# Optimization experiments

Hardware: AMD Instinct MI355X
Metric: run time of the kernel (lower is better)

## Reference

```python
import jax, jax.numpy as jnp
import numpy as np

T, B, Y = 256, 2048, 20   # time, batch, y_dim
H = 256                   # rnn_macro_dim
HD = 256                  # h_dim (decoder MLP)
N_LAYERS = 2


def _gru_cell(x, h, Wih, Whh, bih, bhh):
    # PyTorch GRU cell. Wih: [3H, in], Whh: [3H, H]; gate order r, z, n.
    gx = x @ Wih.T + bih            # [B, 3H]
    gh = h @ Whh.T + bhh            # [B, 3H]
    gx_r, gx_z, gx_n = jnp.split(gx, 3, axis=-1)
    gh_r, gh_z, gh_n = jnp.split(gh, 3, axis=-1)
    r = jax.nn.sigmoid(gx_r + gh_r)
    z = jax.nn.sigmoid(gx_z + gh_z)
    n = jnp.tanh(gx_n + r * gh_n)
    return (1.0 - z) * n + z * h


def setup_inputs() -> dict:
    key = jax.random.key(0)
    ks = jax.random.split(key, 16)
    s = 0.05
    inp = {
        'data': jax.random.normal(ks[0], (T, B, Y), dtype=jnp.float32),
        # GRU layer 0 (input Y) and layer 1 (input H)
        'Wih0': jax.random.normal(ks[1], (3 * H, Y), dtype=jnp.float32) * s,
        'Whh0': jax.random.normal(ks[2], (3 * H, H), dtype=jnp.float32) * s,
        'bih0': jax.random.normal(ks[3], (3 * H,), dtype=jnp.float32) * s,
        'bhh0': jax.random.normal(ks[4], (3 * H,), dtype=jnp.float32) * s,
        'Wih1': jax.random.normal(ks[5], (3 * H, H), dtype=jnp.float32) * s,
        'Whh1': jax.random.normal(ks[6], (3 * H, H), dtype=jnp.float32) * s,
        'bih1': jax.random.normal(ks[7], (3 * H,), dtype=jnp.float32) * s,
        'bhh1': jax.random.normal(ks[8], (3 * H,), dtype=jnp.float32) * s,
        # dec_macro: Linear(H, HD) -> ReLU -> Linear(HD, HD) -> ReLU -> Linear(HD, Y)
        'W1': jax.random.normal(ks[9], (HD, H), dtype=jnp.float32) * s,
        'b1': jax.random.normal(ks[10], (HD,), dtype=jnp.float32) * s,
        'W2': jax.random.normal(ks[11], (HD, HD), dtype=jnp.float32) * s,
        'b2': jax.random.normal(ks[12], (HD,), dtype=jnp.float32) * s,
        'W3': jax.random.normal(ks[13], (Y, HD), dtype=jnp.float32) * s,
        'b3': jax.random.normal(ks[14], (Y,), dtype=jnp.float32) * s,
    }
    return inp


def reference(data, Wih0, Whh0, bih0, bhh0, Wih1, Whh1, bih1, bhh1,
              W1, b1, W2, b2, W3, b3):
    # hp['train'] == 'macro' branch of PROG_RNN_DET.forward
    batch = data.shape[1]
    h_init = jnp.zeros((N_LAYERS, batch, H), dtype=data.dtype)

    def step(h, xs):
        x_t, next_t = xs
        h0 = _gru_cell(x_t, h[0], Wih0, Whh0, bih0, bhh0)
        h1 = _gru_cell(h0, h[1], Wih1, Whh1, bih1, bhh1)
        d = jax.nn.relu(h1 @ W1.T + b1)
        d = jax.nn.relu(d @ W2.T + b2)
        d = d @ W3.T + b3
        loss_t = jnp.sum((d - next_t) ** 2)
        return jnp.stack([h0, h1]), loss_t

    _, losses = jax.lax.scan(step, h_init, (data[:-1], data[1:]))
    return jnp.sum(losses)
```

## Files before the change

kernel.cpp:

```cpp
#include <hip/hip_runtime.h>
#include <stdint.h>

typedef __attribute__((ext_vector_type(4))) float f32x4;
typedef __attribute__((ext_vector_type(2))) long lx2;
typedef unsigned short u16;
typedef unsigned char u8;

#define MFMA8(a,b,c) __builtin_amdgcn_mfma_f32_16x16x32_fp8_fp8((a),(b),(c),0,0,0)

static constexpr int T_STEPS = 256;
static constexpr int BATCH   = 2048;
static constexpr int YDIM    = 20;
static constexpr int BS      = 16;
static constexpr int NWG     = BATCH / BS;

static constexpr int NPAIR   = 768;
static constexpr int WS_U16  = NPAIR * 512;

__device__ __forceinline__ float sigm(float x) { return 1.0f / (1.0f + __expf(-x)); }
__device__ __forceinline__ float tanh_fast(float x) {
    float s = __expf(-2.0f * fabsf(x));
    float r = (1.0f - s) / (1.0f + s);
    return copysignf(r, x);
}
__device__ __forceinline__ f32x4 zero4() { f32x4 v = {0.f,0.f,0.f,0.f}; return v; }
__device__ __forceinline__ u8 f2f8(float v) {
    return (u8)(__builtin_amdgcn_cvt_pk_fp8_f32(v, v, 0, false) & 0xff);
}

__device__ float sval(int P, int half, int l16, int k8,
                      const float* __restrict__ Wih0, const float* __restrict__ Whh0,
                      const float* __restrict__ Wih1, const float* __restrict__ Whh1,
                      const float* __restrict__ W1,   const float* __restrict__ W2,
                      const float* __restrict__ W3) {
    if (P < 192) { int kb=P/24, r=P%24, g=r>>3, wv=r&7, c=wv+8*half;
        return Whh0[(g*256 + c*16 + l16)*256 + kb*32 + k8]; }
    if (P < 224) { int r=P-192; if (r>=24) return 0.f;
        int g=r>>3, wv=r&7, c=wv+8*half, row=g*256+c*16+l16;
        return (k8 < YDIM) ? Wih0[row*YDIM + k8] : 0.f; }
    if (P < 416) { int r=P-224, kb=r/24, rr=r%24, g=rr>>3, wv=rr&7, c=wv+8*half;
        return Whh1[(g*256 + c*16 + l16)*256 + kb*32 + k8]; }
    if (P < 608) { int r=P-416, kb=r/24, rr=r%24, g=rr>>3, wv=rr&7, c=wv+8*half;
        return Wih1[(g*256 + c*16 + l16)*256 + kb*32 + k8]; }
    if (P < 672) { int r=P-608, kb=r>>3, wv=r&7, row=(wv+8*half)*16+l16;
        return W1[row*256 + kb*32 + k8]; }
    if (P < 736) { int r=P-672, kb=r>>3, wv=r&7, row=(wv+8*half)*16+l16;
        return W2[row*256 + kb*32 + k8]; }
    { int r=P-736, s=r>>3, wv=r&7;
      if (wv < 2) { int kb = 2*s + half, row = wv*16 + l16;
          return (row < YDIM) ? W3[row*256 + kb*32 + k8] : 0.f; }
      return 0.f; }
}

__global__ void prep_kernel(const float* __restrict__ Wih0, const float* __restrict__ Whh0,
                            const float* __restrict__ Wih1, const float* __restrict__ Whh1,
                            const float* __restrict__ W1,   const float* __restrict__ W2,
                            const float* __restrict__ W3,   u16* __restrict__ ws,
                            float* __restrict__ out) {
    int tid = blockIdx.x * blockDim.x + threadIdx.x;
    if (tid == 0) out[0] = 0.0f;
    int stride = gridDim.x * blockDim.x;
    for (int m = tid; m < WS_U16; m += stride) {
        int byte0 = 2 * m;
        int P = byte0 >> 10, rem = byte0 & 1023;
        int L = rem >> 4, half = (rem >> 3) & 1, j0 = rem & 7;
        int l16 = L & 15, kqb = (L >> 4) * 8;
        float v0 = sval(P, half, l16, kqb + j0,     Wih0, Whh0, Wih1, Whh1, W1, W2, W3);
        float v1 = sval(P, half, l16, kqb + j0 + 1, Wih0, Whh0, Wih1, Whh1, W1, W2, W3);
        ws[m] = (u16)(__builtin_amdgcn_cvt_pk_fp8_f32(v0, v1, 0, false) & 0xffff);
    }
}

#define BARX() do {                                                 \
    asm volatile("s_waitcnt lgkmcnt(0)" ::: "memory");              \
    __builtin_amdgcn_sched_barrier(0);                              \
    __builtin_amdgcn_s_barrier();                                   \
    __builtin_amdgcn_sched_barrier(0);                              \
} while (0)

#define GM2(ACC, A, PV) do { ACC[0] = MFMA8((A), (PV).x, ACC[0]);   \
                             ACC[1] = MFMA8((A), (PV).y, ACC[1]); } while (0)
#define AFB(S, KT) (*(const long*)&(S)[l16][(KT) * 32 + kq8])
#define LOADC(R0, R1, R2, R3, C) do {                               \
    const u8* b_ = wsl + (size_t)(C) * 32768 + woff;                \
    R0 = *(const lx2*)(b_);          R1 = *(const lx2*)(b_ + 8192); \
    R2 = *(const lx2*)(b_ + 16384); R3 = *(const lx2*)(b_ + 24576); \
} while (0)
#define LP(BASE, P) (*(const lx2*)&(BASE)[(size_t)(P) * 1024 + (size_t)lane * 16])
#define XCH_A(P0,P1,P2,P3, S, KB, AR,AZ,AN) do {                    \
    const long a0_ = AFB(S, KB), a1_ = AFB(S, (KB)+1);              \
    GM2(AR,a0_,P0); GM2(AZ,a0_,P1); GM2(AN,a0_,P2); GM2(AR,a1_,P3); } while (0)
#define XCH_B(P0,P1,P2,P3, S, KB, AR,AZ,AN) do {                    \
    const long a0_ = AFB(S, KB), a1_ = AFB(S, (KB)+1);              \
    GM2(AZ,a0_,P0); GM2(AN,a0_,P1); GM2(AR,a1_,P2); GM2(AZ,a1_,P3); } while (0)
#define XCH_C(P0,P1,P2,P3, S, KB, AR,AZ,AN) do {                    \
    const long a0_ = AFB(S, KB), a1_ = AFB(S, (KB)+1);              \
    GM2(AN,a0_,P0); GM2(AR,a1_,P1); GM2(AZ,a1_,P2); GM2(AN,a1_,P3); } while (0)
#define XCH_M(P0,P1,P2,P3, S, KB0) do {                             \
    const long m0_ = AFB(S, KB0),     m1_ = AFB(S, (KB0)+1);        \
    const long m2_ = AFB(S, (KB0)+2), m3_ = AFB(S, (KB0)+3);        \
    d0 = MFMA8(m0_, P0.x, d0);  d1v = MFMA8(m0_, P0.y, d1v);        \
    d0 = MFMA8(m1_, P1.x, d0);  d1v = MFMA8(m1_, P1.y, d1v);        \
    d0 = MFMA8(m2_, P2.x, d0);  d1v = MFMA8(m2_, P2.y, d1v);        \
    d0 = MFMA8(m3_, P3.x, d0);  d1v = MFMA8(m3_, P3.y, d1v);        \
} while (0)
#define COMBINE(HSH, HR, BRv, BZv, BXNv, BHNv, AR, AZ, AXN, AHN) do {            \
    _Pragma("unroll") for (int jj = 0; jj < 2; ++jj) {                           \
        const int colb_ = (w + 8 * jj) * 16 + l16;                               \
        _Pragma("unroll") for (int q = 0; q < 4; ++q) {                          \
            const float r_ = sigm(AR[jj][q] + BRv[jj]);                          \
            const float z_ = sigm(AZ[jj][q] + BZv[jj]);                          \
            const float n_ = tanh_fast(AXN[jj][q] + BXNv[jj] + r_ * (AHN[jj][q] + BHNv[jj])); \
            const float hn_ = (1.0f - z_) * n_ + z_ * HR[jj][q];                 \
            HR[jj][q] = hn_;                                                     \
            HSH[kq * 4 + q][colb_] = f2f8(hn_); } }                              \
} while (0)
#define DWRITE(DSH, SB) do {                                                     \
    _Pragma("unroll") for (int q = 0; q < 4; ++q) {                              \
        DSH[kq * 4 + q][w * 16 + l16]       = f2f8(fmaxf(d0[q]  + SB[0], 0.f));  \
        DSH[kq * 4 + q][(8 + w) * 16 + l16] = f2f8(fmaxf(d1v[q] + SB[1], 0.f)); }\
} while (0)
#define ZACC(A) do { A[0] = zero4(); A[1] = zero4(); } while (0)

__global__ __launch_bounds__(512, 1) void rnn_main(
    const float* __restrict__ data,
    const float* __restrict__ bih0g, const float* __restrict__ bhh0g,
    const float* __restrict__ bih1g, const float* __restrict__ bhh1g,
    const float* __restrict__ b1g,  const float* __restrict__ b2g,
    const float* __restrict__ b3g,
    const u16* __restrict__ ws, float* __restrict__ out)
{
    __shared__ __align__(16) u8 lds_whh0[3 * 32768];
    __shared__ __align__(16) u8 sh_h0[2][16][272];
    __shared__ __align__(16) u8 sh_h1[2][16][272];
    __shared__ __align__(16) u8 sh_d1[16][272];
    __shared__ __align__(16) u8 sh_d2[16][272];
    __shared__ __align__(16) u8 sh_x[16][32];

    const int tid  = threadIdx.x;
    const int w    = tid >> 6;
    const int lane = tid & 63;
    const int l16  = lane & 15;
    const int kq   = lane >> 4;
    const int kq8  = kq * 8;
    const int b0   = blockIdx.x * BS;
    const int xr   = tid / YDIM, xc = tid - xr * YDIM;
    const size_t woff = (size_t)w * 1024 + (size_t)lane * 16;

    {
        const lx2* s = (const lx2*)ws;
        lx2* dW = (lx2*)lds_whh0;
        for (int i = tid; i < 6144; i += 512) dW[i] = s[i];
    }

    for (int i = tid; i < 2 * 16 * 272; i += 512) { (&sh_h0[0][0][0])[i] = 0; (&sh_h1[0][0][0])[i] = 0; }
    for (int i = tid; i < 16 * 32;  i += 512) (&sh_x[0][0])[i] = 0;
    if (tid < BS * YDIM) sh_x[xr][xc] = f2f8(data[(size_t)b0 * YDIM + tid]);

    float bR0[2], bZ0[2], bXN0[2], bHN0[2], bR1[2], bZ1[2], bXN1[2], bHN1[2], s1r[2], s2r[2];
    #pragma unroll
    for (int jj = 0; jj < 2; ++jj) {
        const int colb = (w + 8 * jj) * 16 + l16;
        bR0[jj]  = bih0g[colb] + bhh0g[colb];
        bZ0[jj]  = bih0g[colb + 256] + bhh0g[colb + 256];
        bXN0[jj] = bih0g[colb + 512];  bHN0[jj] = bhh0g[colb + 512];
        bR1[jj]  = bih1g[colb] + bhh1g[colb];
        bZ1[jj]  = bih1g[colb + 256] + bhh1g[colb + 256];
        bXN1[jj] = bih1g[colb + 512];  bHN1[jj] = bhh1g[colb + 512];
        s1r[jj]  = b1g[colb];  s2r[jj] = b2g[colb];
    }
    float s3r = 0.0f;
    { const int col = w * 16 + l16; if (w < 2 && col < YDIM) s3r = b3g[col]; }

    float hr0[2][4] = {{0,0,0,0},{0,0,0,0}};
    float hr1[2][4] = {{0,0,0,0},{0,0,0,0}};
    f32x4 r0[2], z0[2], xn0[2], hn0[2];
    f32x4 r1[2], z1[2], xn1[2], hn1[2];
    f32x4 d0, d1v;
    lx2 p00, p01, p02, p03, p10, p11, p12, p13, p20, p21, p22, p23;

    __syncthreads();

    {
        const u8* wsl = (const u8*)ws;
        LOADC(p00, p01, p02, p03, 3);
        LOADC(p10, p11, p12, p13, 4);
        LOADC(p20, p21, p22, p23, 5);
    }
    float loss = 0.0f;

    #pragma unroll 1
    for (int t = 0; t < T_STEPS - 1; ++t) {
        const u8* wsl = (const u8*)ws;
        asm volatile("" : "+s"(wsl));
        u8 (*h0o)[272] = sh_h0[t & 1];  u8 (*h0n)[272] = sh_h0[(t & 1) ^ 1];
        u8 (*h1o)[272] = sh_h1[t & 1];  u8 (*h1n)[272] = sh_h1[(t & 1) ^ 1];

        ZACC(r0); ZACC(z0); ZACC(xn0); ZACC(hn0);
        ZACC(r1); ZACC(z1); ZACC(xn1); ZACC(hn1);

        {   lx2 q0=LP(lds_whh0, w),    q1=LP(lds_whh0, 8+w),  q2=LP(lds_whh0, 16+w), q3=LP(lds_whh0, 24+w);
            XCH_A(q0,q1,q2,q3, h0o, 0, r0,z0,hn0); }
        {   lx2 q0=LP(lds_whh0, 32+w), q1=LP(lds_whh0, 40+w), q2=LP(lds_whh0, 48+w), q3=LP(lds_whh0, 56+w);
            XCH_B(q0,q1,q2,q3, h0o, 1, r0,z0,hn0); }
        {   lx2 q0=LP(lds_whh0, 64+w), q1=LP(lds_whh0, 72+w), q2=LP(lds_whh0, 80+w), q3=LP(lds_whh0, 88+w);
            XCH_C(q0,q1,q2,q3, h0o, 2, r0,z0,hn0); }
        XCH_A(p00,p01,p02,p03, h0o, 4, r0,z0,hn0);  LOADC(p00,p01,p02,p03, 6);
        XCH_B(p10,p11,p12,p13, h0o, 5, r0,z0,hn0);  LOADC(p10,p11,p12,p13, 7);
        XCH_C(p20,p21,p22,p23, h0o, 6, r0,z0,hn0);  LOADC(p20,p21,p22,p23, 8);
        {
            const long ax = *(const long*)&sh_x[l16][kq8];
            GM2(r0, ax, p00); GM2(z0, ax, p01); GM2(xn0, ax, p02);
        }
        LOADC(p00,p01,p02,p03, 9);
        XCH_A(p10,p11,p12,p13, h1o, 0, r1,z1,hn1);  LOADC(p10,p11,p12,p13, 10);
        XCH_B(p20,p21,p22,p23, h1o, 1, r1,z1,hn1);  LOADC(p20,p21,p22,p23, 11);
        XCH_C(p00,p01,p02,p03, h1o, 2, r1,z1,hn1);  LOADC(p00,p01,p02,p03, 12);
        XCH_A(p10,p11,p12,p13, h1o, 4, r1,z1,hn1);  LOADC(p10,p11,p12,p13, 13);
        XCH_B(p20,p21,p22,p23, h1o, 5, r1,z1,hn1);  LOADC(p20,p21,p22,p23, 14);
        XCH_C(p00,p01,p02,p03, h1o, 6, r1,z1,hn1);  LOADC(p00,p01,p02,p03, 15);
        COMBINE(h0n, hr0, bR0, bZ0, bXN0, bHN0, r0, z0, xn0, hn0);
        BARX();
        XCH_A(p10,p11,p12,p13, h0n, 0, r1,z1,xn1);  LOADC(p10,p11,p12,p13, 16);
        XCH_B(p20,p21,p22,p23, h0n, 1, r1,z1,xn1);  LOADC(p20,p21,p22,p23, 17);
        XCH_C(p00,p01,p02,p03, h0n, 2, r1,z1,xn1);  LOADC(p00,p01,p02,p03, 18);
        XCH_A(p10,p11,p12,p13, h0n, 4, r1,z1,xn1);  LOADC(p10,p11,p12,p13, 19);
        XCH_B(p20,p21,p22,p23, h0n, 5, r1,z1,xn1);  LOADC(p20,p21,p22,p23, 20);
        XCH_C(p00,p01,p02,p03, h0n, 6, r1,z1,xn1);  LOADC(p00,p01,p02,p03, 21);
        COMBINE(h1n, hr1, bR1, bZ1, bXN1, bHN1, r1, z1, xn1, hn1);
        BARX();
        d0 = zero4(); d1v = zero4();
        float xv = 0.f, tg0 = 0.f, tg1 = 0.f, tg2 = 0.f, tg3 = 0.f;
        {
            const float* tp = data + (size_t)(t + 1) * (BATCH * YDIM) + (size_t)b0 * YDIM;
            if (tid < BS * YDIM) xv = tp[tid];
            if (w < 2) {
                const int col = w * 16 + l16;
                if (col < YDIM) {
                    tg0 = tp[(kq * 4 + 0) * YDIM + col];
                    tg1 = tp[(kq * 4 + 1) * YDIM + col];
                    tg2 = tp[(kq * 4 + 2) * YDIM + col];
                    tg3 = tp[(kq * 4 + 3) * YDIM + col];
                }
            }
        }
        XCH_M(p10,p11,p12,p13, h1n, 0);  LOADC(p10,p11,p12,p13, 22);
        XCH_M(p20,p21,p22,p23, h1n, 4);  LOADC(p20,p21,p22,p23, 23);
        DWRITE(sh_d1, s1r);
        if (tid < BS * YDIM) sh_x[xr][xc] = f2f8(xv);
        BARX();
        d0 = zero4(); d1v = zero4();
        XCH_M(p00,p01,p02,p03, sh_d1, 0);  LOADC(p00,p01,p02,p03, 3);
        XCH_M(p10,p11,p12,p13, sh_d1, 4);  LOADC(p10,p11,p12,p13, 4);
        DWRITE(sh_d2, s2r);
        BARX();
        if (w < 2) {
            f32x4 lacc = zero4();
            lacc = MFMA8(AFB(sh_d2, 0), p20.x, lacc);
            lacc = MFMA8(AFB(sh_d2, 1), p20.y, lacc);
            lacc = MFMA8(AFB(sh_d2, 2), p21.x, lacc);
            lacc = MFMA8(AFB(sh_d2, 3), p21.y, lacc);
            lacc = MFMA8(AFB(sh_d2, 4), p22.x, lacc);
            lacc = MFMA8(AFB(sh_d2, 5), p22.y, lacc);
            lacc = MFMA8(AFB(sh_d2, 6), p23.x, lacc);
            lacc = MFMA8(AFB(sh_d2, 7), p23.y, lacc);
            const int col = w * 16 + l16;
            if (col < YDIM) {
                const float e0 = lacc[0] + s3r - tg0;
                const float e1 = lacc[1] + s3r - tg1;
                const float e2 = lacc[2] + s3r - tg2;
                const float e3 = lacc[3] + s3r - tg3;
                loss += e0 * e0 + e1 * e1 + e2 * e2 + e3 * e3;
            }
        }
        LOADC(p20,p21,p22,p23, 5);
    }

    asm volatile("s_waitcnt vmcnt(0)" ::: "memory");
    #pragma unroll
    for (int s = 32; s > 0; s >>= 1) loss += __shfl_down(loss, s, 64);
    if (lane == 0 && w < 2) atomicAdd(out, loss);
}

extern "C" void kernel_launch(void* const* d_in, const int* in_sizes, int n_in,
                              void* d_out, int out_size, void* d_ws, size_t ws_size,
                              hipStream_t stream) {
    const float* data = (const float*)d_in[0];
    const float* Wih0 = (const float*)d_in[1];
    const float* Whh0 = (const float*)d_in[2];
    const float* bih0 = (const float*)d_in[3];
    const float* bhh0 = (const float*)d_in[4];
    const float* Wih1 = (const float*)d_in[5];
    const float* Whh1 = (const float*)d_in[6];
    const float* bih1 = (const float*)d_in[7];
    const float* bhh1 = (const float*)d_in[8];
    const float* W1   = (const float*)d_in[9];
    const float* b1   = (const float*)d_in[10];
    const float* W2   = (const float*)d_in[11];
    const float* b2   = (const float*)d_in[12];
    const float* W3   = (const float*)d_in[13];
    const float* b3   = (const float*)d_in[14];
    u16*   ws  = (u16*)d_ws;
    float* out = (float*)d_out;

    hipLaunchKernelGGL(prep_kernel, dim3(512), dim3(256), 0, stream,
                       Wih0, Whh0, Wih1, Whh1, W1, W2, W3, ws, out);
    hipLaunchKernelGGL(rnn_main, dim3(NWG), dim3(512), 0, stream,
                       data, bih0, bhh0, bih1, bhh1, b1, b2, b3, ws, out);
}
```

Baseline: 2.120 ms.

## Process 32 batch rows per workgroup with 1024 threads sharing LDS weights

Measured after the change: 4.088 ms. 92.8% more time.

```diff
diff --git a/kernel.cpp b/kernel.cpp
--- a/kernel.cpp
+++ b/kernel.cpp
@@ -11,7 +11,7 @@
 static constexpr int T_STEPS = 256;
 static constexpr int BATCH   = 2048;
 static constexpr int YDIM    = 20;
-static constexpr int BS      = 16;
+static constexpr int BS      = 32;
 static constexpr int NWG     = BATCH / BS;
 
 static constexpr int NPAIR   = 768;
@@ -80,7 +80,7 @@
 
 #define GM2(ACC, A, PV) do { ACC[0] = MFMA8((A), (PV).x, ACC[0]);   \
                              ACC[1] = MFMA8((A), (PV).y, ACC[1]); } while (0)
-#define AFB(S, KT) (*(const long*)&(S)[l16][(KT) * 32 + kq8])
+#define AFB(S, KT) (*(const long*)&(S)[rowoff + l16][(KT) * 32 + kq8])
 #define LOADC(R0, R1, R2, R3, C) do {                               \
     const u8* b_ = wsl + (size_t)(C) * 32768 + woff;                \
     R0 = *(const lx2*)(b_);          R1 = *(const lx2*)(b_ + 8192); \
@@ -106,23 +106,23 @@
 } while (0)
 #define COMBINE(HSH, HR, BRv, BZv, BXNv, BHNv, AR, AZ, AXN, AHN) do {            \
     _Pragma("unroll") for (int jj = 0; jj < 2; ++jj) {                           \
-        const int colb_ = (w + 8 * jj) * 16 + l16;                               \
+        const int colb_ = (wl + 8 * jj) * 16 + l16;                              \
         _Pragma("unroll") for (int q = 0; q < 4; ++q) {                          \
             const float r_ = sigm(AR[jj][q] + BRv[jj]);                          \
             const float z_ = sigm(AZ[jj][q] + BZv[jj]);                          \
             const float n_ = tanh_fast(AXN[jj][q] + BXNv[jj] + r_ * (AHN[jj][q] + BHNv[jj])); \
             const float hn_ = (1.0f - z_) * n_ + z_ * HR[jj][q];                 \
             HR[jj][q] = hn_;                                                     \
-            HSH[kq * 4 + q][colb_] = f2f8(hn_); } }                              \
+            HSH[rowoff + kq * 4 + q][colb_] = f2f8(hn_); } }                     \
 } while (0)
 #define DWRITE(DSH, SB) do {                                                     \
     _Pragma("unroll") for (int q = 0; q < 4; ++q) {                              \
-        DSH[kq * 4 + q][w * 16 + l16]       = f2f8(fmaxf(d0[q]  + SB[0], 0.f));  \
-        DSH[kq * 4 + q][(8 + w) * 16 + l16] = f2f8(fmaxf(d1v[q] + SB[1], 0.f)); }\
+        DSH[rowoff + kq * 4 + q][wl * 16 + l16]       = f2f8(fmaxf(d0[q]  + SB[0], 0.f)); \
+        DSH[rowoff + kq * 4 + q][(8 + wl) * 16 + l16] = f2f8(fmaxf(d1v[q] + SB[1], 0.f)); } \
 } while (0)
 #define ZACC(A) do { A[0] = zero4(); A[1] = zero4(); } while (0)
 
-__global__ __launch_bounds__(512, 1) void rnn_main(
+__global__ __launch_bounds__(1024, 1) void rnn_main(
     const float* __restrict__ data,
     const float* __restrict__ bih0g, const float* __restrict__ bhh0g,
     const float* __restrict__ bih1g, const float* __restrict__ bhh1g,
@@ -131,36 +131,38 @@
     const u16* __restrict__ ws, float* __restrict__ out)
 {
     __shared__ __align__(16) u8 lds_whh0[3 * 32768];
-    __shared__ __align__(16) u8 sh_h0[2][16][272];
-    __shared__ __align__(16) u8 sh_h1[2][16][272];
-    __shared__ __align__(16) u8 sh_d1[16][272];
-    __shared__ __align__(16) u8 sh_d2[16][272];
-    __shared__ __align__(16) u8 sh_x[16][32];
-
-    const int tid  = threadIdx.x;
-    const int w    = tid >> 6;
-    const int lane = tid & 63;
-    const int l16  = lane & 15;
-    const int kq   = lane >> 4;
-    const int kq8  = kq * 8;
-    const int b0   = blockIdx.x * BS;
-    const int xr   = tid / YDIM, xc = tid - xr * YDIM;
-    const size_t woff = (size_t)w * 1024 + (size_t)lane * 16;
+    __shared__ __align__(16) u8 sh_h0[2][32][272];
+    __shared__ __align__(16) u8 sh_h1[2][32][272];
+    __shared__ __align__(16) u8 sh_d1[32][272];
+    __shared__ __align__(16) u8 sh_d2[32][272];
+    __shared__ __align__(16) u8 sh_x[32][32];
+
+    const int tid    = threadIdx.x;
+    const int w      = tid >> 6;
+    const int wl     = w & 7;
+    const int rowoff = (w >> 3) * 16;
+    const int lane   = tid & 63;
+    const int l16    = lane & 15;
+    const int kq     = lane >> 4;
+    const int kq8    = kq * 8;
+    const int b0     = blockIdx.x * BS;
+    const int xr     = tid / YDIM, xc = tid - xr * YDIM;
+    const size_t woff = (size_t)wl * 1024 + (size_t)lane * 16;
 
     {
         const lx2* s = (const lx2*)ws;
         lx2* dW = (lx2*)lds_whh0;
-        for (int i = tid; i < 6144; i += 512) dW[i] = s[i];
-    }
-
-    for (int i = tid; i < 2 * 16 * 272; i += 512) { (&sh_h0[0][0][0])[i] = 0; (&sh_h1[0][0][0])[i] = 0; }
-    for (int i = tid; i < 16 * 32;  i += 512) (&sh_x[0][0])[i] = 0;
+        for (int i = tid; i < 6144; i += 1024) dW[i] = s[i];
+    }
+
+    for (int i = tid; i < 2 * 32 * 272; i += 1024) { (&sh_h0[0][0][0])[i] = 0; (&sh_h1[0][0][0])[i] = 0; }
+    for (int i = tid; i < 32 * 32;  i += 1024) (&sh_x[0][0])[i] = 0;
     if (tid < BS * YDIM) sh_x[xr][xc] = f2f8(data[(size_t)b0 * YDIM + tid]);
 
     float bR0[2], bZ0[2], bXN0[2], bHN0[2], bR1[2], bZ1[2], bXN1[2], bHN1[2], s1r[2], s2r[2];
     #pragma unroll
     for (int jj = 0; jj < 2; ++jj) {
-        const int colb = (w + 8 * jj) * 16 + l16;
+        const int colb = (wl + 8 * jj) * 16 + l16;
         bR0[jj]  = bih0g[colb] + bhh0g[colb];
         bZ0[jj]  = bih0g[colb + 256] + bhh0g[colb + 256];
         bXN0[jj] = bih0g[colb + 512];  bHN0[jj] = bhh0g[colb + 512];
@@ -170,7 +172,7 @@
         s1r[jj]  = b1g[colb];  s2r[jj] = b2g[colb];
     }
     float s3r = 0.0f;
-    { const int col = w * 16 + l16; if (w < 2 && col < YDIM) s3r = b3g[col]; }
+    { const int col = wl * 16 + l16; if (wl < 2 && col < YDIM) s3r = b3g[col]; }
 
     float hr0[2][4] = {{0,0,0,0},{0,0,0,0}};
     float hr1[2][4] = {{0,0,0,0},{0,0,0,0}};
@@ -199,17 +201,17 @@
         ZACC(r0); ZACC(z0); ZACC(xn0); ZACC(hn0);
         ZACC(r1); ZACC(z1); ZACC(xn1); ZACC(hn1);
 
-        {   lx2 q0=LP(lds_whh0, w),    q1=LP(lds_whh0, 8+w),  q2=LP(lds_whh0, 16+w), q3=LP(lds_whh0, 24+w);
+        {   lx2 q0=LP(lds_whh0, wl),    q1=LP(lds_whh0, 8+wl),  q2=LP(lds_whh0, 16+wl), q3=LP(lds_whh0, 24+wl);
             XCH_A(q0,q1,q2,q3, h0o, 0, r0,z0,hn0); }
-        {   lx2 q0=LP(lds_whh0, 32+w), q1=LP(lds_whh0, 40+w), q2=LP(lds_whh0, 48+w), q3=LP(lds_whh0, 56+w);
+        {   lx2 q0=LP(lds_whh0, 32+wl), q1=LP(lds_whh0, 40+wl), q2=LP(lds_whh0, 48+wl), q3=LP(lds_whh0, 56+wl);
             XCH_B(q0,q1,q2,q3, h0o, 1, r0,z0,hn0); }
-        {   lx2 q0=LP(lds_whh0, 64+w), q1=LP(lds_whh0, 72+w), q2=LP(lds_whh0, 80+w), q3=LP(lds_whh0, 88+w);
+        {   lx2 q0=LP(lds_whh0, 64+wl), q1=LP(lds_whh0, 72+wl), q2=LP(lds_whh0, 80+wl), q3=LP(lds_whh0, 88+wl);
             XCH_C(q0,q1,q2,q3, h0o, 2, r0,z0,hn0); }
         XCH_A(p00,p01,p02,p03, h0o, 4, r0,z0,hn0);  LOADC(p00,p01,p02,p03, 6);
         XCH_B(p10,p11,p12,p13, h0o, 5, r0,z0,hn0);  LOADC(p10,p11,p12,p13, 7);
         XCH_C(p20,p21,p22,p23, h0o, 6, r0,z0,hn0);  LOADC(p20,p21,p22,p23, 8);
         {
-            const long ax = *(const long*)&sh_x[l16][kq8];
+            const long ax = *(const long*)&sh_x[rowoff + l16][kq8];
             GM2(r0, ax, p00); GM2(z0, ax, p01); GM2(xn0, ax, p02);
         }
         LOADC(p00,p01,p02,p03, 9);
@@ -234,13 +236,13 @@
         {
             const float* tp = data + (size_t)(t + 1) * (BATCH * YDIM) + (size_t)b0 * YDIM;
             if (tid < BS * YDIM) xv = tp[tid];
-            if (w < 2) {
-                const int col = w * 16 + l16;
+            if (wl < 2) {
+                const int col = wl * 16 + l16;
                 if (col < YDIM) {
-                    tg0 = tp[(kq * 4 + 0) * YDIM + col];
-                    tg1 = tp[(kq * 4 + 1) * YDIM + col];
-                    tg2 = tp[(kq * 4 + 2) * YDIM + col];
-                    tg3 = tp[(kq * 4 + 3) * YDIM + col];
+                    tg0 = tp[(rowoff + kq * 4 + 0) * YDIM + col];
+                    tg1 = tp[(rowoff + kq * 4 + 1) * YDIM + col];
+                    tg2 = tp[(rowoff + kq * 4 + 2) * YDIM + col];
+                    tg3 = tp[(rowoff + kq * 4 + 3) * YDIM + col];
                 }
             }
         }
@@ -254,7 +256,7 @@
         XCH_M(p10,p11,p12,p13, sh_d1, 4);  LOADC(p10,p11,p12,p13, 4);
         DWRITE(sh_d2, s2r);
         BARX();
-        if (w < 2) {
+        if (wl < 2) {
             f32x4 lacc = zero4();
             lacc = MFMA8(AFB(sh_d2, 0), p20.x, lacc);
             lacc = MFMA8(AFB(sh_d2, 1), p20.y, lacc);
@@ -264,7 +266,7 @@
             lacc = MFMA8(AFB(sh_d2, 5), p22.y, lacc);
             lacc = MFMA8(AFB(sh_d2, 6), p23.x, lacc);
             lacc = MFMA8(AFB(sh_d2, 7), p23.y, lacc);
-            const int col = w * 16 + l16;
+            const int col = wl * 16 + l16;
             if (col < YDIM) {
                 const float e0 = lacc[0] + s3r - tg0;
                 const float e1 = lacc[1] + s3r - tg1;
@@ -279,7 +281,7 @@
     asm volatile("s_waitcnt vmcnt(0)" ::: "memory");
     #pragma unroll
     for (int s = 32; s > 0; s >>= 1) loss += __shfl_down(loss, s, 64);
-    if (lane == 0 && w < 2) atomicAdd(out, loss);
+    if (lane == 0 && wl < 2) atomicAdd(out, loss);
 }
 
 extern "C" void kernel_launch(void* const* d_in, const int* in_sizes, int n_in,
@@ -305,6 +307,6 @@
 
     hipLaunchKernelGGL(prep_kernel, dim3(512), dim3(256), 0, stream,
                        Wih0, Whh0, Wih1, Whh1, W1, W2, W3, ws, out);
-    hipLaunchKernelGGL(rnn_main, dim3(NWG), dim3(512), 0, stream,
+    hipLaunchKernelGGL(rnn_main, dim3(NWG), dim3(1024), 0, stream,
                        data, bih0, bhh0, bih1, bhh1, b1, b2, b3, ws, out);
 }
```
